# Kernel tuning notes

Hardware: AMD Instinct MI355X
Metric: run time of the kernel (lower is better)

The kernel has to match this reference:

```python
import jax, jax.numpy as jnp
import numpy as np

B, L, H, N, VOCAB, OUT, NL = 16, 2048, 512, 64, 256, 256, 4
N2 = N // 2  # conjugate-symmetric half of the state


def setup_inputs() -> dict:
    key = jax.random.key(0)
    ks = jax.random.split(key, 8)
    x = jax.random.randint(ks[0], (B, L), 0, VOCAB)
    emb = jax.random.normal(ks[1], (VOCAB, H), jnp.float32)
    Ws = jax.random.normal(ks[2], (NL, H, H), jnp.float32) / np.float32(np.sqrt(H))
    bs = jnp.zeros((NL, H), jnp.float32)
    dt_min, dt_max = 1e-3, 1e-1
    log_dt = (jax.random.uniform(ks[3], (NL, H), jnp.float32)
              * np.float32(np.log(dt_max) - np.log(dt_min)) + np.float32(np.log(dt_min)))
    log_A_real = jnp.full((NL, H, N2), np.float32(np.log(0.5)), jnp.float32)
    A_imag = jnp.broadcast_to(np.float32(np.pi) * jnp.arange(N2, dtype=jnp.float32), (NL, H, N2))
    C_re = jax.random.normal(ks[4], (NL, H, N2), jnp.float32)
    C_im = jax.random.normal(ks[5], (NL, H, N2), jnp.float32)
    Ds = jax.random.normal(ks[6], (NL, H), jnp.float32)
    Wo = jax.random.normal(ks[7], (H, OUT), jnp.float32) / np.float32(np.sqrt(H))
    bo = jnp.zeros((OUT,), jnp.float32)
    return dict(x=x, emb=emb, Ws=Ws, bs=bs, log_dt=log_dt, log_A_real=log_A_real,
                A_imag=A_imag, C_re=C_re, C_im=C_im, Ds=Ds, Wo=Wo, bo=bo)


def _s4d(u, log_dt, log_A_real, A_imag, C_re, C_im, D):
    # u: (B, Lseq, H). Standard minimal S4D (diagonal SSM, ZOH-style kernel, FFT causal conv).
    Lseq = u.shape[1]
    dt = jnp.exp(log_dt)                      # (H,)
    A = -jnp.exp(log_A_real) + 1j * A_imag    # (H, N2) complex
    C = C_re + 1j * C_im                      # (H, N2)
    dtA = A * dt[:, None]                     # (H, N2)
    coef = C * (jnp.exp(dtA) - 1.0) / A       # (H, N2)
    # Vandermonde over time: exp(dtA * l), l = 0..L-1
    vand = jnp.exp(dtA[:, :, None] * jnp.arange(Lseq, dtype=jnp.float32))  # (H, N2, L)
    K = 2.0 * jnp.einsum('hn,hnl->hl', coef, vand).real                    # (H, L)
    ud = jnp.transpose(u, (0, 2, 1))          # (B, H, L)
    kf = jnp.fft.rfft(K, n=2 * Lseq)
    uf = jnp.fft.rfft(ud, n=2 * Lseq)
    y = jnp.fft.irfft(uf * kf, n=2 * Lseq)[..., :Lseq]  # causal conv
    y = y + D[:, None] * ud                   # skip connection
    return jnp.transpose(y, (0, 2, 1))        # (B, L, H)


def reference(x, emb, Ws, bs, log_dt, log_A_real, A_imag, C_re, C_im, Ds, Wo, bo):
    h = emb[x]  # (B, L, H)
    for i in range(NL):
        # every sub-layer gets the outer residual: x = layer(x) + x
        h = (h @ Ws[i] + bs[i]) + h           # Linear + residual
        h = jax.nn.relu(h) + h                # ReLU + residual
        h = h + h                             # Dropout (eval: identity) + residual
        h = _s4d(h, log_dt[i], log_A_real[i], A_imag[i], C_re[i], C_im[i], Ds[i]) + h
        h = jax.nn.relu(h) + h
        h = h + h
    return h @ Wo + bo
```

## Files before the change

kernel.cpp:

```cpp
#include <hip/hip_runtime.h>

#define BB 16
#define LL 2048
#define HH 512
#define NN2 32
#define NLAY 4
#define OUTD 256
#define BLM (BB*LL)
#define NELEM ((size_t)BLM*HH)
#define NC 8
#define LC (LL/NC)

typedef __attribute__((ext_vector_type(8))) short s8v;
typedef __attribute__((ext_vector_type(4))) float f4v;

__device__ __forceinline__ unsigned short f2bf(float f) {
  unsigned u = __float_as_uint(f);
  return (unsigned short)((u + 0x7fffu + ((u >> 16) & 1u)) >> 16);
}
__device__ __forceinline__ float bf2f(unsigned short h) {
  return __uint_as_float((unsigned)h << 16);
}
__device__ __forceinline__ void gload16(const void* g, void* l) {
  __builtin_amdgcn_global_load_lds(
      (const __attribute__((address_space(1))) unsigned int*)g,
      (__attribute__((address_space(3))) unsigned int*)l, 16, 0, 0);
}

__global__ __launch_bounds__(256) void k_embed(const int* __restrict__ x,
    const float* __restrict__ emb, unsigned short* __restrict__ Ahi,
    unsigned short* __restrict__ Alo) {
  int idx = blockIdx.x * 256 + threadIdx.x;
  int j4 = idx & 127;
  int bl = idx >> 7;
  int tok = x[bl];
  float4 v = reinterpret_cast<const float4*>(emb)[tok * 128 + j4];
  unsigned short h0 = f2bf(v.x), h1 = f2bf(v.y), h2 = f2bf(v.z), h3 = f2bf(v.w);
  unsigned short l0 = f2bf(v.x - bf2f(h0)), l1 = f2bf(v.y - bf2f(h1));
  unsigned short l2 = f2bf(v.z - bf2f(h2)), l3 = f2bf(v.w - bf2f(h3));
  uint2 hp = make_uint2((unsigned)h0 | ((unsigned)h1 << 16),
                        (unsigned)h2 | ((unsigned)h3 << 16));
  uint2 lp = make_uint2((unsigned)l0 | ((unsigned)l1 << 16),
                        (unsigned)l2 | ((unsigned)l3 << 16));
  *reinterpret_cast<uint2*>(&Ahi[(size_t)idx * 4]) = hp;
  *reinterpret_cast<uint2*>(&Alo[(size_t)idx * 4]) = lp;
}

__global__ __launch_bounds__(256) void k_trans(const float* __restrict__ W, int N,
    unsigned short* __restrict__ th, unsigned short* __restrict__ tl) {
  int t = blockIdx.x * 256 + threadIdx.x;
  int k = t & 511, n = t >> 9;
  float v = W[(size_t)k * N + n];
  unsigned short hi = f2bf(v);
  th[(size_t)n * 512 + k] = hi;
  tl[(size_t)n * 512 + k] = f2bf(v - bf2f(hi));
}

__global__ __launch_bounds__(256) void k_params(const float* __restrict__ log_dt,
    const float* __restrict__ log_A_real, const float* __restrict__ A_imag,
    const float* __restrict__ C_re, const float* __restrict__ C_im,
    int layer, float4* __restrict__ par) {
  int idx = blockIdx.x * 256 + threadIdx.x;
  int h = idx >> 5;
  int o = layer * HH * NN2 + idx;
  float dt  = expf(log_dt[layer * HH + h]);
  float Are = -expf(log_A_real[o]);
  float Aim = A_imag[o];
  float er = expf(Are * dt);
  float lr = er * cosf(Aim * dt), li = er * sinf(Aim * dt);
  float inv  = 1.0f / (Are * Are + Aim * Aim);
  float numr = lr - 1.0f, numi = li;
  float qr = (numr * Are + numi * Aim) * inv;
  float qi = (numi * Are - numr * Aim) * inv;
  float cr = C_re[o], ci = C_im[o];
  par[idx] = make_float4(lr, li, 2.0f * (cr * qr - ci * qi),
                                 2.0f * (cr * qi + ci * qr));
}

template<int EPI>
__global__ __launch_bounds__(256) void k_gemm(
    const unsigned short* __restrict__ Ahi, const unsigned short* __restrict__ Alo,
    const unsigned short* __restrict__ Bhi, const unsigned short* __restrict__ Blo,
    const float* __restrict__ bias, float* __restrict__ Out, int N) {
  __shared__ short lds[16384];
  const int tid = threadIdx.x;
  const int lane = tid & 63, w = tid >> 6;
  const int wr = w >> 1, wc = w & 1;
  const int m0 = blockIdx.y * 128, n0 = blockIdx.x * 128;
  const int lm = lane & 15, lk = lane >> 4;

  const unsigned short* ga[2][2]; const unsigned short* gb[2][2];
  short *da[2][2], *db[2][2];
#pragma unroll
  for (int f2 = 0; f2 < 2; ++f2) {
    int f = w * 2 + f2;
    size_t ra = (size_t)(m0 + f * 16 + lm) * 512 + lk * 8;
    size_t rb = (size_t)(n0 + f * 16 + lm) * 512 + lk * 8;
    ga[0][f2] = Ahi + ra; ga[1][f2] = Alo + ra;
    gb[0][f2] = Bhi + rb; gb[1][f2] = Blo + rb;
    da[0][f2] = &lds[f * 512 + lane * 8];
    da[1][f2] = &lds[4096 + f * 512 + lane * 8];
    db[0][f2] = &lds[8192 + f * 512 + lane * 8];
    db[1][f2] = &lds[12288 + f * 512 + lane * 8];
  }
  f4v acc[4][4];
#pragma unroll
  for (int i = 0; i < 4; ++i)
#pragma unroll
    for (int j = 0; j < 4; ++j) acc[i][j] = (f4v){0.f, 0.f, 0.f, 0.f};

  for (int kt = 0; kt < 16; ++kt) {
#pragma unroll
    for (int f2 = 0; f2 < 2; ++f2) {
      gload16(ga[0][f2] + kt * 32, da[0][f2]);
      gload16(ga[1][f2] + kt * 32, da[1][f2]);
      gload16(gb[0][f2] + kt * 32, db[0][f2]);
      gload16(gb[1][f2] + kt * 32, db[1][f2]);
    }
    __syncthreads();
    s8v ah[4], al[4], bh[4], bl[4];
#pragma unroll
    for (int i = 0; i < 4; ++i) {
      ah[i] = *(const s8v*)&lds[(wr * 4 + i) * 512 + lane * 8];
      al[i] = *(const s8v*)&lds[4096 + (wr * 4 + i) * 512 + lane * 8];
      bh[i] = *(const s8v*)&lds[8192 + (wc * 4 + i) * 512 + lane * 8];
      bl[i] = *(const s8v*)&lds[12288 + (wc * 4 + i) * 512 + lane * 8];
    }
#pragma unroll
    for (int mi = 0; mi < 4; ++mi)
#pragma unroll
      for (int ni = 0; ni < 4; ++ni) {
        acc[mi][ni] = __builtin_amdgcn_mfma_f32_16x16x32_bf16(ah[mi], bh[ni], acc[mi][ni], 0, 0, 0);
        acc[mi][ni] = __builtin_amdgcn_mfma_f32_16x16x32_bf16(al[mi], bh[ni], acc[mi][ni], 0, 0, 0);
        acc[mi][ni] = __builtin_amdgcn_mfma_f32_16x16x32_bf16(ah[mi], bl[ni], acc[mi][ni], 0, 0, 0);
      }
    __syncthreads();
  }
  float bb[4];
#pragma unroll
  for (int ni = 0; ni < 4; ++ni) bb[ni] = bias[n0 + wc * 64 + ni * 16 + lm];
#pragma unroll
  for (int mi = 0; mi < 4; ++mi) {
#pragma unroll
    for (int r = 0; r < 4; ++r) {
      int row = m0 + wr * 64 + mi * 16 + lk * 4 + r;
      float* po = Out + (size_t)row * N;
      const unsigned short* ph = Ahi + (size_t)row * 512;
      const unsigned short* pl = Alo + (size_t)row * 512;
#pragma unroll
      for (int ni = 0; ni < 4; ++ni) {
        int col = n0 + wc * 64 + ni * 16 + lm;
        float t = acc[mi][ni][r] + bb[ni];
        if (EPI) {
          t += bf2f(ph[col]) + bf2f(pl[col]);
          t = t < 0.f ? 2.f * t : 4.f * t;
        }
        po[col] = t;
      }
    }
  }
}

__global__ __launch_bounds__(256) void k_sa(const float* __restrict__ U,
    const float4* __restrict__ par, float2* __restrict__ st) {
  int tid = threadIdx.x;
  int n = tid & 31, hs = tid >> 5;
  int hb = blockIdx.x, c = blockIdx.y, b = blockIdx.z;
  int h = (hb << 3) + hs;
  float4 p = par[(h << 5) + n];
  float lr = p.x, li = p.y;
  const float* Up = U + ((size_t)b * LL + (size_t)c * LC) * HH + h;
  float sr = 0.f, si = 0.f;
  auto step = [&](float uv) {
    float nsr = fmaf(lr, sr, fmaf(-li, si, uv));
    si = fmaf(lr, si, li * sr);
    sr = nsr;
  };
  float u0 = Up[0], u1 = Up[HH], u2 = Up[2 * HH], u3 = Up[3 * HH];
  for (int lg = 0; lg < LC / 4; ++lg) {
    const float* nx = Up + (size_t)(lg * 4 + 4) * HH;
    float v0 = nx[0], v1 = nx[HH], v2 = nx[2 * HH], v3 = nx[3 * HH];
    step(u0); step(u1); step(u2); step(u3);
    u0 = v0; u1 = v1; u2 = v2; u3 = v3;
  }
  st[(((size_t)b * 7 + c) * HH + h) * NN2 + n] = make_float2(sr, si);
}

__global__ __launch_bounds__(256) void k_fold(const float4* __restrict__ par,
    float2* __restrict__ st) {
  int t = blockIdx.x * 256 + threadIdx.x;
  int hn = t & 16383;
  int b = t >> 14;
  float4 p = par[hn];
  float ar = p.x, ai = p.y;
#pragma unroll
  for (int s = 0; s < 8; ++s) { float nr = ar * ar - ai * ai; ai = 2.f * ar * ai; ar = nr; }
  float gr = 0.f, gi = 0.f;
  size_t idx = (size_t)b * 7 * 16384 + hn;
  for (int c = 0; c < 7; ++c) {
    float2 s = st[idx + (size_t)c * 16384];
    float ngr = fmaf(ar, gr, fmaf(-ai, gi, s.x));
    gi = fmaf(ar, gi, fmaf(ai, gr, s.y));
    gr = ngr;
    st[idx + (size_t)c * 16384] = make_float2(gr, gi);
  }
}

__global__ __launch_bounds__(256) void k_sb(const float* __restrict__ U,
    const float4* __restrict__ par, const float2* __restrict__ st,
    const float* __restrict__ D, unsigned short* __restrict__ Hhi,
    unsigned short* __restrict__ Hlo) {
  int tid = threadIdx.x;
  int q = tid & 3, hs = tid >> 2;
  int hb = blockIdx.x, c = blockIdx.y, b = blockIdx.z;
  int h = (hb << 6) + hs;
  float lr[8], li[8], cr[8], ci[8], tr[8], ti[8];
#pragma unroll
  for (int j = 0; j < 8; ++j) {
    float4 p = par[(h << 5) + (q << 3) + j];
    lr[j] = p.x; li[j] = p.y; cr[j] = p.z; ci[j] = p.w;
    tr[j] = 0.f; ti[j] = 0.f;
  }
  if (c > 0) {
#pragma unroll
    for (int j = 0; j < 8; ++j) {
      float2 s = st[(((size_t)b * 7 + (c - 1)) * HH + h) * NN2 + (q << 3) + j];
      tr[j] = cr[j] * s.x - ci[j] * s.y;
      ti[j] = cr[j] * s.y + ci[j] * s.x;
    }
  }
  float dp1 = D[h] + 1.0f;
  size_t base = ((size_t)b * LL + (size_t)c * LC) * HH + h;
  const float* Up = U + base;
  auto step = [&](float uv) -> float {
    float ys = 0.f;
#pragma unroll
    for (int j = 0; j < 8; ++j) {
      float ntr = fmaf(lr[j], tr[j], fmaf(-li[j], ti[j], cr[j] * uv));
      ti[j] = fmaf(lr[j], ti[j], fmaf(li[j], tr[j], ci[j] * uv));
      tr[j] = ntr;
      ys += ntr;
    }
    ys += __shfl_xor(ys, 1);
    ys += __shfl_xor(ys, 2);
    float t4 = fmaf(dp1, uv, ys);
    return t4 < 0.f ? 2.f * t4 : 4.f * t4;
  };
  float u0 = Up[0], u1 = Up[HH], u2 = Up[2 * HH], u3 = Up[3 * HH];
  for (int lg = 0; lg < LC / 4; ++lg) {
    const float* nx = Up + (size_t)(lg * 4 + 4) * HH;
    float v0 = nx[0], v1 = nx[HH], v2 = nx[2 * HH], v3 = nx[3 * HH];
    float r0 = step(u0), r1 = step(u1), r2 = step(u2), r3 = step(u3);
    float rq = q == 0 ? r0 : q == 1 ? r1 : q == 2 ? r2 : r3;
    size_t o = base + (size_t)(lg * 4 + q) * HH;
    unsigned short hi = f2bf(rq);
    Hhi[o] = hi;
    Hlo[o] = f2bf(rq - bf2f(hi));
    u0 = v0; u1 = v1; u2 = v2; u3 = v3;
  }
}

extern "C" void kernel_launch(void* const* d_in, const int* in_sizes, int n_in,
                              void* d_out, int out_size, void* d_ws, size_t ws_size,
                              hipStream_t stream) {
  const int*   x      = (const int*)d_in[0];
  const float* emb    = (const float*)d_in[1];
  const float* Ws     = (const float*)d_in[2];
  const float* bs     = (const float*)d_in[3];
  const float* log_dt = (const float*)d_in[4];
  const float* lAr    = (const float*)d_in[5];
  const float* Aim    = (const float*)d_in[6];
  const float* Cre    = (const float*)d_in[7];
  const float* Cim    = (const float*)d_in[8];
  const float* Ds     = (const float*)d_in[9];
  const float* Wo     = (const float*)d_in[10];
  const float* bo     = (const float*)d_in[11];

  float*          bufU   = (float*)d_ws;
  unsigned short* bufAhi = (unsigned short*)(bufU + NELEM);
  unsigned short* bufAlo = bufAhi + NELEM;
  float4*         par    = (float4*)(bufAlo + NELEM);
  float2*         st     = (float2*)(par + HH * NN2);
  unsigned short* wth    = (unsigned short*)(st + (size_t)BB * 7 * HH * NN2);
  unsigned short* wtl    = wth + 512 * 512;

  k_embed<<<(int)(NELEM / 4 / 256), 256, 0, stream>>>(x, emb, bufAhi, bufAlo);
  for (int i = 0; i < NLAY; ++i) {
    k_params<<<HH * NN2 / 256, 256, 0, stream>>>(log_dt, lAr, Aim, Cre, Cim, i, par);
    k_trans<<<HH * 512 / 256, 256, 0, stream>>>(Ws + (size_t)i * HH * HH, HH, wth, wtl);
    k_gemm<1><<<dim3(HH / 128, BLM / 128), 256, 0, stream>>>(
        bufAhi, bufAlo, wth, wtl, bs + i * HH, bufU, HH);
    k_sa<<<dim3(64, 7, BB), 256, 0, stream>>>(bufU, par, st);
    k_fold<<<BB * HH * NN2 / 256, 256, 0, stream>>>(par, st);
    k_sb<<<dim3(8, NC, BB), 256, 0, stream>>>(bufU, par, st, Ds + i * HH, bufAhi, bufAlo);
  }
  k_trans<<<OUTD * 512 / 256, 256, 0, stream>>>(Wo, OUTD, wth, wtl);
  k_gemm<0><<<dim3(OUTD / 128, BLM / 128), 256, 0, stream>>>(
      bufAhi, bufAlo, wth, wtl, bo, (float*)d_out, OUTD);
}
```

Baseline: 1.210 ms.

## Double-buffer GEMM LDS tiles and split the scan into more chunks

The GEMM now uses two LDS buffers, so the global-to-LDS loads for the next K tile are issued while MFMAs run on the current tile. This hides load latency, at the cost of doubling LDS per block, which may lower occupancy. Separately, the chunked SSM scan goes from 8 to 16 chunks, giving the scan kernels twice the parallelism and half the serial chunk length. In exchange, the fold step now covers 15 chunks and needs more state storage.

```diff
diff --git a/kernel.cpp b/kernel.cpp
--- a/kernel.cpp
+++ b/kernel.cpp
@@ -8,8 +8,9 @@
 #define OUTD 256
 #define BLM (BB*LL)
 #define NELEM ((size_t)BLM*HH)
-#define NC 8
+#define NC 16
 #define LC (LL/NC)
+#define LGLC 7
 
 typedef __attribute__((ext_vector_type(8))) short s8v;
 typedef __attribute__((ext_vector_type(4))) float f4v;
@@ -82,7 +83,7 @@
     const unsigned short* __restrict__ Ahi, const unsigned short* __restrict__ Alo,
     const unsigned short* __restrict__ Bhi, const unsigned short* __restrict__ Blo,
     const float* __restrict__ bias, float* __restrict__ Out, int N) {
-  __shared__ short lds[16384];
+  __shared__ short lds[32768];
   const int tid = threadIdx.x;
   const int lane = tid & 63, w = tid >> 6;
   const int wr = w >> 1, wc = w & 1;
@@ -109,22 +110,23 @@
 #pragma unroll
     for (int j = 0; j < 4; ++j) acc[i][j] = (f4v){0.f, 0.f, 0.f, 0.f};
 
-  for (int kt = 0; kt < 16; ++kt) {
+  auto stage = [&](int kt, int bofs) {
 #pragma unroll
     for (int f2 = 0; f2 < 2; ++f2) {
-      gload16(ga[0][f2] + kt * 32, da[0][f2]);
-      gload16(ga[1][f2] + kt * 32, da[1][f2]);
-      gload16(gb[0][f2] + kt * 32, db[0][f2]);
-      gload16(gb[1][f2] + kt * 32, db[1][f2]);
-    }
-    __syncthreads();
+      gload16(ga[0][f2] + kt * 32, da[0][f2] + bofs);
+      gload16(ga[1][f2] + kt * 32, da[1][f2] + bofs);
+      gload16(gb[0][f2] + kt * 32, db[0][f2] + bofs);
+      gload16(gb[1][f2] + kt * 32, db[1][f2] + bofs);
+    }
+  };
+  auto compute = [&](int bofs) {
     s8v ah[4], al[4], bh[4], bl[4];
 #pragma unroll
     for (int i = 0; i < 4; ++i) {
-      ah[i] = *(const s8v*)&lds[(wr * 4 + i) * 512 + lane * 8];
-      al[i] = *(const s8v*)&lds[4096 + (wr * 4 + i) * 512 + lane * 8];
-      bh[i] = *(const s8v*)&lds[8192 + (wc * 4 + i) * 512 + lane * 8];
-      bl[i] = *(const s8v*)&lds[12288 + (wc * 4 + i) * 512 + lane * 8];
+      ah[i] = *(const s8v*)&lds[bofs + (wr * 4 + i) * 512 + lane * 8];
+      al[i] = *(const s8v*)&lds[bofs + 4096 + (wr * 4 + i) * 512 + lane * 8];
+      bh[i] = *(const s8v*)&lds[bofs + 8192 + (wc * 4 + i) * 512 + lane * 8];
+      bl[i] = *(const s8v*)&lds[bofs + 12288 + (wc * 4 + i) * 512 + lane * 8];
     }
 #pragma unroll
     for (int mi = 0; mi < 4; ++mi)
@@ -134,6 +136,17 @@
         acc[mi][ni] = __builtin_amdgcn_mfma_f32_16x16x32_bf16(al[mi], bh[ni], acc[mi][ni], 0, 0, 0);
         acc[mi][ni] = __builtin_amdgcn_mfma_f32_16x16x32_bf16(ah[mi], bl[ni], acc[mi][ni], 0, 0, 0);
       }
+  };
+
+  stage(0, 0);
+  __syncthreads();
+#pragma unroll 1
+  for (int t = 0; t < 8; ++t) {
+    stage(2 * t + 1, 16384);
+    compute(0);
+    __syncthreads();
+    if (t < 7) stage(2 * t + 2, 0);
+    compute(16384);
     __syncthreads();
   }
   float bb[4];
@@ -183,7 +196,7 @@
     step(u0); step(u1); step(u2); step(u3);
     u0 = v0; u1 = v1; u2 = v2; u3 = v3;
   }
-  st[(((size_t)b * 7 + c) * HH + h) * NN2 + n] = make_float2(sr, si);
+  st[(((size_t)b * (NC - 1) + c) * HH + h) * NN2 + n] = make_float2(sr, si);
 }
 
 __global__ __launch_bounds__(256) void k_fold(const float4* __restrict__ par,
@@ -194,10 +207,10 @@
   float4 p = par[hn];
   float ar = p.x, ai = p.y;
 #pragma unroll
-  for (int s = 0; s < 8; ++s) { float nr = ar * ar - ai * ai; ai = 2.f * ar * ai; ar = nr; }
+  for (int s = 0; s < LGLC; ++s) { float nr = ar * ar - ai * ai; ai = 2.f * ar * ai; ar = nr; }
   float gr = 0.f, gi = 0.f;
-  size_t idx = (size_t)b * 7 * 16384 + hn;
-  for (int c = 0; c < 7; ++c) {
+  size_t idx = (size_t)b * (NC - 1) * 16384 + hn;
+  for (int c = 0; c < NC - 1; ++c) {
     float2 s = st[idx + (size_t)c * 16384];
     float ngr = fmaf(ar, gr, fmaf(-ai, gi, s.x));
     gi = fmaf(ar, gi, fmaf(ai, gr, s.y));
@@ -224,7 +237,7 @@
   if (c > 0) {
 #pragma unroll
     for (int j = 0; j < 8; ++j) {
-      float2 s = st[(((size_t)b * 7 + (c - 1)) * HH + h) * NN2 + (q << 3) + j];
+      float2 s = st[(((size_t)b * (NC - 1) + (c - 1)) * HH + h) * NN2 + (q << 3) + j];
       tr[j] = cr[j] * s.x - ci[j] * s.y;
       ti[j] = cr[j] * s.y + ci[j] * s.x;
     }
@@ -281,7 +294,7 @@
   unsigned short* bufAlo = bufAhi + NELEM;
   float4*         par    = (float4*)(bufAlo + NELEM);
   float2*         st     = (float2*)(par + HH * NN2);
-  unsigned short* wth    = (unsigned short*)(st + (size_t)BB * 7 * HH * NN2);
+  unsigned short* wth    = (unsigned short*)(st + (size_t)BB * (NC - 1) * HH * NN2);
   unsigned short* wtl    = wth + 512 * 512;
 
   k_embed<<<(int)(NELEM / 4 / 256), 256, 0, stream>>>(x, emb, bufAhi, bufAlo);
@@ -290,7 +303,7 @@
     k_trans<<<HH * 512 / 256, 256, 0, stream>>>(Ws + (size_t)i * HH * HH, HH, wth, wtl);
     k_gemm<1><<<dim3(HH / 128, BLM / 128), 256, 0, stream>>>(
         bufAhi, bufAlo, wth, wtl, bs + i * HH, bufU, HH);
-    k_sa<<<dim3(64, 7, BB), 256, 0, stream>>>(bufU, par, st);
+    k_sa<<<dim3(64, NC - 1, BB), 256, 0, stream>>>(bufU, par, st);
     k_fold<<<BB * HH * NN2 / 256, 256, 0, stream>>>(par, st);
     k_sb<<<dim3(8, NC, BB), 256, 0, stream>>>(bufU, par, st, Ds + i * HH, bufAhi, bufAlo);
   }
```

Result: no change. 1.189 ms (-1.8%).
